# Performance work log

Measured on AMD Instinct MI355X. Metric: run time of the kernel, lower is better.

Reference implementation:

```python
import jax, jax.numpy as jnp
import numpy as np

MARGIN = 0.3
NEG_FILL = 1e9  # larger than any real distance; keeps min-reduction valid


def setup_inputs() -> dict:
    key = jax.random.key(0)
    k1, k2 = jax.random.split(key)
    embeddings = jax.random.normal(k1, (4096, 256), dtype=jnp.float32)
    labels = jax.random.randint(k2, (4096,), 0, 512, dtype=jnp.int64)
    return {"embeddings": embeddings, "labels": labels}


def _pairwise_distances(embeddings):
    # Faithful to the torch version, including the zero-distance sqrt guard.
    dot = jnp.matmul(embeddings, embeddings.T)          # [B, B]
    sq = jnp.diagonal(dot)                              # [B]
    d2 = sq[None, :] - 2.0 * dot + sq[:, None]
    d2 = jnp.maximum(d2, 0.0)
    zero_mask = (d2 == 0.0).astype(embeddings.dtype)
    d = jnp.sqrt(d2 + zero_mask * 1e-16)
    return d * (1.0 - zero_mask)


def reference(embeddings, labels):
    B = labels.shape[0]
    d = _pairwise_distances(embeddings)                 # [B, B]

    same = labels[:, None] == labels[None, :]           # [B, B]
    eye = jnp.eye(B, dtype=bool)
    pos_mask = same & ~eye
    neg_mask = ~same

    has_pos = jnp.any(pos_mask, axis=1)
    has_neg = jnp.any(neg_mask, axis=1)
    valid = has_pos & has_neg                           # [B]

    # Row-wise masked reductions (distances >= 0 so -1 is a safe max fill).
    hardest_pos = jnp.max(jnp.where(pos_mask, d, -1.0), axis=1)
    hardest_neg = jnp.min(jnp.where(neg_mask, d, NEG_FILL), axis=1)

    per_anchor = jnp.maximum(hardest_pos - hardest_neg + MARGIN, 0.0)
    n_valid = jnp.sum(valid.astype(jnp.float32))
    total = jnp.sum(jnp.where(valid, per_anchor, 0.0))
    return jnp.where(n_valid > 0, total / jnp.maximum(n_valid, 1.0), 0.0)
```

## Files before the change

kernel.cpp:

```cpp
#include <hip/hip_runtime.h>
#include <hip/hip_fp16.h>

#define BN 4096
#define DIM 256
#define PANEL 4104
#define NBLK 32
#define NPAIR 528
#define MARGIN_F 0.3f
#define NEG_FILL_F 1e9f
#define HP_SENT_BITS 0xBF800000

typedef __attribute__((ext_vector_type(8))) _Float16 f16x8;
typedef __attribute__((ext_vector_type(4))) float f32x4;

__global__ __launch_bounds__(256) void tl_prep(const float* __restrict__ E,
                                               float* __restrict__ norms,
                                               float* __restrict__ red,
                                               ushort* __restrict__ Eh) {
    __shared__ ushort sh[4][272];
    const int tid  = threadIdx.x;
    const int lane = tid & 63;
    const int wrow = tid >> 6;
    const int row0 = blockIdx.x * 4;
    const int row  = row0 + wrow;

    float4 v = reinterpret_cast<const float4*>(E + (size_t)row * DIM)[lane];
    float f[4] = {v.x, v.y, v.z, v.w};
    ushort hb[4];
    float s = 0.0f;
    #pragma unroll
    for (int q = 0; q < 4; ++q) {
        s += f[q] * f[q];
        hb[q] = __half_as_ushort(__float2half(f[q]));
    }
    *reinterpret_cast<ushort4*>(&sh[wrow][lane * 4]) = make_ushort4(hb[0], hb[1], hb[2], hb[3]);

    #pragma unroll
    for (int m = 32; m; m >>= 1) s += __shfl_xor(s, m, 64);
    if (lane == 0) norms[row] = s;
    if (blockIdx.x == 0 && tid < 3) red[tid] = 0.0f;

    __syncthreads();
    if (tid < 128) {
        const int kc = tid >> 2, r = tid & 3;
        const f16x8 frag = *reinterpret_cast<const f16x8*>(&sh[r][kc * 8]);
        *reinterpret_cast<f16x8*>(Eh + (((size_t)(kc * PANEL + row0 + r)) << 3)) = frag;
    }
}

__global__ __launch_bounds__(256, 4) void tl_main(const ushort* __restrict__ Eh,
                                                  const int* __restrict__ labels,
                                                  const float* __restrict__ norms,
                                                  float* __restrict__ pHP,
                                                  float* __restrict__ pHN) {
    __shared__ int comb[512];

    const int tid  = threadIdx.x;
    const int lane = tid & 63;
    const int wave = tid >> 6;
    const int wy = wave >> 1, wx = wave & 1;
    const int quad = lane >> 4, l15 = lane & 15;

    int t = blockIdx.x, ib = 0, off = 0;
    while (off + (NBLK - ib) <= t) { off += NBLK - ib; ++ib; }
    const int jb = ib + (t - off);
    const int i0 = ib * 128, j0 = jb * 128;

    f32x4 acc[4][4];
    #pragma unroll
    for (int r = 0; r < 4; ++r)
        #pragma unroll
        for (int c = 0; c < 4; ++c)
            acc[r][c] = (f32x4){0.f, 0.f, 0.f, 0.f};

    const ushort* baseQ = Eh + (size_t)quad * (PANEL * 8);
    int rA[4], rB[4];
    #pragma unroll
    for (int r = 0; r < 4; ++r) rA[r] = (i0 + wy * 64 + r * 16 + l15) * 8;
    #pragma unroll
    for (int c = 0; c < 4; ++c) rB[c] = (j0 + wx * 64 + c * 16 + l15) * 8;

    #pragma unroll
    for (int s = 0; s < 8; ++s) {
        const size_t so = (size_t)s * (4u * PANEL * 8u);
        f16x8 a[4], b[4];
        #pragma unroll
        for (int r = 0; r < 4; ++r)
            a[r] = *reinterpret_cast<const f16x8*>(baseQ + so + (size_t)rA[r]);
        #pragma unroll
        for (int c = 0; c < 4; ++c)
            b[c] = *reinterpret_cast<const f16x8*>(baseQ + so + (size_t)rB[c]);
        #pragma unroll
        for (int c = 0; c < 4; ++c)
            #pragma unroll
            for (int r = 0; r < 4; ++r)
                acc[r][c] = __builtin_amdgcn_mfma_f32_16x16x32_f16(a[r], b[c], acc[r][c], 0, 0, 0);
    }

    const int rowBase = i0 + wy * 64;
    const int colBase = j0 + wx * 64;

    int*      srhp = comb;
    unsigned* srhn = reinterpret_cast<unsigned*>(comb + 128);
    int*      schp = comb + 256;
    unsigned* schn = reinterpret_cast<unsigned*>(comb + 384);
    if (tid < 128) {
        srhp[tid] = (int)HP_SENT_BITS;
        srhn[tid] = __float_as_uint(NEG_FILL_F);
        schp[tid] = (int)HP_SENT_BITS;
        schn[tid] = __float_as_uint(NEG_FILL_F);
    }
    __syncthreads();

    float ncol[4]; int lcol[4];
    #pragma unroll
    for (int c = 0; c < 4; ++c) {
        const int g = colBase + c * 16 + l15;
        ncol[c] = norms[g];
        lcol[c] = labels[g];
    }
    float cmax[4], cmin[4];
    #pragma unroll
    for (int c = 0; c < 4; ++c) { cmax[c] = -1.0f; cmin[c] = NEG_FILL_F; }

    #pragma unroll
    for (int r = 0; r < 4; ++r) {
        float nrow[4]; int lrow[4];
        #pragma unroll
        for (int e = 0; e < 4; ++e) {
            const int g = rowBase + r * 16 + quad * 4 + e;
            nrow[e] = norms[g];
            lrow[e] = labels[g];
        }
        float rmax[4], rmin[4];
        #pragma unroll
        for (int e = 0; e < 4; ++e) { rmax[e] = -1.0f; rmin[e] = NEG_FILL_F; }

        #pragma unroll
        for (int c = 0; c < 4; ++c) {
            const int gcol = colBase + c * 16 + l15;
            #pragma unroll
            for (int e = 0; e < 4; ++e) {
                const int grow = rowBase + r * 16 + quad * 4 + e;
                float d2 = nrow[e] + ncol[c] - 2.0f * acc[r][c][e];
                d2 = fmaxf(d2, 0.0f);
                if (lrow[e] == lcol[c]) {
                    if (grow != gcol) {
                        rmax[e] = fmaxf(rmax[e], d2);
                        cmax[c] = fmaxf(cmax[c], d2);
                    }
                } else {
                    rmin[e] = fminf(rmin[e], d2);
                    cmin[c] = fminf(cmin[c], d2);
                }
            }
        }
        #pragma unroll
        for (int m = 1; m <= 8; m <<= 1) {
            #pragma unroll
            for (int e = 0; e < 4; ++e) {
                rmax[e] = fmaxf(rmax[e], __shfl_xor(rmax[e], m, 64));
                rmin[e] = fminf(rmin[e], __shfl_xor(rmin[e], m, 64));
            }
        }
        if (l15 == 0) {
            #pragma unroll
            for (int e = 0; e < 4; ++e) {
                const int lr = wy * 64 + r * 16 + quad * 4 + e;
                atomicMax(&srhp[lr], __float_as_int(rmax[e]));
                atomicMin(&srhn[lr], __float_as_uint(rmin[e]));
            }
        }
    }

    #pragma unroll
    for (int m = 16; m <= 32; m <<= 1) {
        #pragma unroll
        for (int c = 0; c < 4; ++c) {
            cmax[c] = fmaxf(cmax[c], __shfl_xor(cmax[c], m, 64));
            cmin[c] = fminf(cmin[c], __shfl_xor(cmin[c], m, 64));
        }
    }
    if (quad == 0) {
        #pragma unroll
        for (int c = 0; c < 4; ++c) {
            const int lc = wx * 64 + c * 16 + l15;
            atomicMax(&schp[lc], __float_as_int(cmax[c]));
            atomicMin(&schn[lc], __float_as_uint(cmin[c]));
        }
    }
    __syncthreads();
    if (tid < 128) {
        float rp = __int_as_float(srhp[tid]);
        float rn = __uint_as_float(srhn[tid]);
        const float cp = __int_as_float(schp[tid]);
        const float cn = __uint_as_float(schn[tid]);
        if (ib == jb) {
            pHP[(size_t)jb * BN + i0 + tid] = fmaxf(rp, cp);
            pHN[(size_t)jb * BN + i0 + tid] = fminf(rn, cn);
        } else {
            pHP[(size_t)jb * BN + i0 + tid] = rp;
            pHN[(size_t)jb * BN + i0 + tid] = rn;
            pHP[(size_t)ib * BN + j0 + tid] = cp;
            pHN[(size_t)ib * BN + j0 + tid] = cn;
        }
    }
}

__global__ __launch_bounds__(256) void tl_reduce(const float* __restrict__ pHP,
                                                 const float* __restrict__ pHN,
                                                 float* __restrict__ red,
                                                 float* __restrict__ out) {
    __shared__ float shp[4][64], shn[4][64];
    const int rl = threadIdx.x & 63;
    const int g  = threadIdx.x >> 6;
    const int i  = blockIdx.x * 64 + rl;
    float hp2 = -1.0f, hn2 = NEG_FILL_F;
    #pragma unroll
    for (int q = 0; q < 8; ++q) {
        const int s = g * 8 + q;
        hp2 = fmaxf(hp2, pHP[(size_t)s * BN + i]);
        hn2 = fminf(hn2, pHN[(size_t)s * BN + i]);
    }
    shp[g][rl] = hp2;
    shn[g][rl] = hn2;
    __syncthreads();
    if (g == 0) {
        #pragma unroll
        for (int k = 1; k < 4; ++k) {
            hp2 = fmaxf(hp2, shp[k][rl]);
            hn2 = fminf(hn2, shn[k][rl]);
        }
        const bool valid = (hp2 >= 0.0f) && (hn2 < NEG_FILL_F);
        const float hp = sqrtf(fmaxf(hp2, 0.0f));
        const float hn = sqrtf(hn2);
        const float per = fmaxf(hp - hn + MARGIN_F, 0.0f);
        float s_ = valid ? per : 0.0f;
        float c_ = valid ? 1.0f : 0.0f;
        #pragma unroll
        for (int m = 32; m; m >>= 1) {
            s_ += __shfl_xor(s_, m, 64);
            c_ += __shfl_xor(c_, m, 64);
        }
        if (rl == 0) {
            atomicAdd(&red[0], s_);
            atomicAdd(&red[1], c_);
            __threadfence();
            const unsigned ticket = atomicAdd(reinterpret_cast<unsigned*>(&red[2]), 1u);
            if (ticket == gridDim.x - 1) {
                const float S2 = atomicAdd(&red[0], 0.0f);
                const float C2 = atomicAdd(&red[1], 0.0f);
                out[0] = (C2 > 0.0f) ? (S2 / fmaxf(C2, 1.0f)) : 0.0f;
            }
        }
    }
}

extern "C" void kernel_launch(void* const* d_in, const int* in_sizes, int n_in,
                              void* d_out, int out_size, void* d_ws, size_t ws_size,
                              hipStream_t stream) {
    const float* E      = (const float*)d_in[0];
    const int*   labels = (const int*)d_in[1];

    float*  ws    = (float*)d_ws;
    float*  norms = ws;
    float*  red   = ws + 4096;
    float*  pHP   = ws + 8192;
    float*  pHN   = ws + 8192 + NBLK * BN;
    ushort* Eh    = (ushort*)(ws + 8192 + 2 * NBLK * BN);

    tl_prep<<<BN / 4, 256, 0, stream>>>(E, norms, red, Eh);
    tl_main<<<NPAIR, 256, 0, stream>>>(Eh, labels, norms, pHP, pHN);
    tl_reduce<<<BN / 64, 256, 0, stream>>>(pHP, pHN, red, (float*)d_out);
}
```

Baseline: 80.16 us.

## Stage GEMM operand panels through double-buffered LDS with direct global-to-LDS loads

Each wave used to load its own A and B fragments straight from global memory, so waves that share rows or columns of the tile fetched the same data again. The block now cooperatively copies each k-step's A and B panels into a two-slot LDS buffer using global_load_lds, and waves read their fragments from LDS. The next step's copy is issued before the current step's MFMAs to overlap load latency with compute. This adds 32 KB of LDS per block and a barrier every k-step, which could reduce occupancy or expose sync stalls.

```diff
diff --git a/kernel.cpp b/kernel.cpp
--- a/kernel.cpp
+++ b/kernel.cpp
@@ -12,6 +12,12 @@
 
 typedef __attribute__((ext_vector_type(8))) _Float16 f16x8;
 typedef __attribute__((ext_vector_type(4))) float f32x4;
+
+__device__ __forceinline__ void gld_lds16(const void* g, void* l) {
+    __builtin_amdgcn_global_load_lds(
+        (const __attribute__((address_space(1))) unsigned int*)g,
+        (__attribute__((address_space(3))) unsigned int*)l, 16, 0, 0);
+}
 
 __global__ __launch_bounds__(256) void tl_prep(const float* __restrict__ E,
                                                float* __restrict__ norms,
@@ -53,6 +59,7 @@
                                                   const float* __restrict__ norms,
                                                   float* __restrict__ pHP,
                                                   float* __restrict__ pHN) {
+    __shared__ __align__(16) ushort smem[2][8192];
     __shared__ int comb[512];
 
     const int tid  = threadIdx.x;
@@ -73,23 +80,38 @@
         for (int c = 0; c < 4; ++c)
             acc[r][c] = (f32x4){0.f, 0.f, 0.f, 0.f};
 
-    const ushort* baseQ = Eh + (size_t)quad * (PANEL * 8);
-    int rA[4], rB[4];
-    #pragma unroll
-    for (int r = 0; r < 4; ++r) rA[r] = (i0 + wy * 64 + r * 16 + l15) * 8;
-    #pragma unroll
-    for (int c = 0; c < 4; ++c) rB[c] = (j0 + wx * 64 + c * 16 + l15) * 8;
-
+    auto stage = [&](int s, int buf) {
+        #pragma unroll
+        for (int c = 0; c < 4; ++c) {
+            const int idx  = c * 256 + tid;
+            const int part = idx >> 9;
+            const int kcl  = (idx >> 7) & 3;
+            const int m    = idx & 127;
+            const int base = part ? j0 : i0;
+            const ushort* src = Eh + (((size_t)((s * 4 + kcl) * PANEL + base + m)) << 3);
+            gld_lds16(src, &smem[buf][idx << 3]);
+        }
+    };
+
+    stage(0, 0);
     #pragma unroll
     for (int s = 0; s < 8; ++s) {
-        const size_t so = (size_t)s * (4u * PANEL * 8u);
+        const int buf = s & 1;
+        __syncthreads();
+        if (s + 1 < 8) stage(s + 1, buf ^ 1);
+
+        const ushort* sb = &smem[buf][0];
         f16x8 a[4], b[4];
         #pragma unroll
-        for (int r = 0; r < 4; ++r)
-            a[r] = *reinterpret_cast<const f16x8*>(baseQ + so + (size_t)rA[r]);
-        #pragma unroll
-        for (int c = 0; c < 4; ++c)
-            b[c] = *reinterpret_cast<const f16x8*>(baseQ + so + (size_t)rB[c]);
+        for (int r = 0; r < 4; ++r) {
+            const int mi = wy * 64 + r * 16 + l15;
+            a[r] = *reinterpret_cast<const f16x8*>(&sb[(quad * 128 + mi) * 8]);
+        }
+        #pragma unroll
+        for (int c = 0; c < 4; ++c) {
+            const int ni = wx * 64 + c * 16 + l15;
+            b[c] = *reinterpret_cast<const f16x8*>(&sb[(512 + quad * 128 + ni) * 8]);
+        }
         #pragma unroll
         for (int c = 0; c < 4; ++c)
             #pragma unroll
```

After: 79.30 us. About the same (-1.1%).
